# Performance work log

Hardware: AMD Instinct MI355X
Metric: run time of the kernel (lower is better)

## Reference

```python
import jax, jax.numpy as jnp
import numpy as np

H = 64  # hidden_dim

def _lstm_layer(x, Wih, Whh, bih, bhh):
    # x: [B,T,D]; Wih: [4H,D]; Whh: [4H,H]; biases: [4H]
    B = x.shape[0]
    xW = jnp.einsum('btd,gd->btg', x, Wih) + (bih + bhh)  # [B,T,4H], fold both biases
    xW = jnp.swapaxes(xW, 0, 1)  # [T,B,4H]
    h0 = jnp.zeros((B, H), x.dtype)
    c0 = jnp.zeros((B, H), x.dtype)

    def step(carry, g_x):
        h, c = carry
        gates = g_x + h @ Whh.T  # [B,4H]; torch gate order i,f,g,o
        i, f, g, o = jnp.split(gates, 4, axis=-1)
        i = jax.nn.sigmoid(i)
        f = jax.nn.sigmoid(f)
        g = jnp.tanh(g)
        o = jax.nn.sigmoid(o)
        c = f * c + i * g
        h = o * jnp.tanh(c)
        return (h, c), h

    (hT, cT), hs = jax.lax.scan(step, (h0, c0), xW)
    return jnp.swapaxes(hs, 0, 1), hT  # [B,T,H], [B,H]


def setup_inputs() -> dict:
    key = jax.random.key(0)
    ks = jax.random.split(key, 14)
    B, T, D = 2048, 1024, 1
    s = 1.0 / np.sqrt(H)  # torch LSTM/Linear init scale
    u = lambda k, shape: jax.random.uniform(k, shape, jnp.float32, -s, s)
    return {
        'x': jax.random.normal(ks[0], (B, T, D), jnp.float32),
        'Wih0': u(ks[1], (4 * H, D)),
        'Whh0': u(ks[2], (4 * H, H)),
        'bih0': u(ks[3], (4 * H,)),
        'bhh0': u(ks[4], (4 * H,)),
        'Wih1': u(ks[5], (4 * H, H)),
        'Whh1': u(ks[6], (4 * H, H)),
        'bih1': u(ks[7], (4 * H,)),
        'bhh1': u(ks[8], (4 * H,)),
        'Wc1': u(ks[9], (H // 2, H)),
        'bc1': u(ks[10], (H // 2,)),
        'Wc2': u(ks[11], (1, H // 2)),
        'bc2': u(ks[12], (1,)),
    }


def reference(x, Wih0, Whh0, bih0, bhh0, Wih1, Whh1, bih1, bhh1, Wc1, bc1, Wc2, bc2):
    # 2-layer unidirectional LSTM (dropout off at inference)
    h1_seq, _ = _lstm_layer(x, Wih0, Whh0, bih0, bhh0)
    _, h_n = _lstm_layer(h1_seq, Wih1, Whh1, bih1, bhh1)  # final hidden of top layer [B,H]
    # classifier head: Linear(H,H//2) -> ReLU -> Linear(H//2,1)
    hid = jax.nn.relu(h_n @ Wc1.T + bc1)
    logits = hid @ Wc2.T + bc2  # [B,1]
    return logits
```

## Files before the change

kernel.cpp:

```cpp
#include <hip/hip_runtime.h>

typedef _Float16 f16;
typedef _Float16 f16x8 __attribute__((ext_vector_type(8)));
typedef float    f32x4 __attribute__((ext_vector_type(4)));
typedef unsigned int       u32;
typedef unsigned long long u64;

#define HD    64
#define GW    16
#define NT    512
#define CHUNK 8
#define XCH   256
#define L2E   1.44269504088896340736f
#define L2E2  2.88539008177792681472f

#define BAR_LGKM() asm volatile("s_waitcnt lgkmcnt(0)\ns_barrier" ::: "memory")

#if __has_builtin(__builtin_amdgcn_exp2f)
#define EXP2(x) __builtin_amdgcn_exp2f(x)
#else
#define EXP2(x) __expf((x) * 0.69314718055994530942f)
#endif

__device__ __forceinline__ f32x4 MFMA(f16x8 a, f16x8 b, f32x4 c) {
    return __builtin_amdgcn_mfma_f32_16x16x32_f16(a, b, c, 0, 0, 0);
}
__device__ __forceinline__ int kinv(int k) {
    int kf = k >> 5, qk = (k >> 3) & 3, j = k & 7;
    int tile = (kf << 3) | (qk << 1) | (j & 1);
    return tile * 4 + (j >> 1);
}
__device__ __forceinline__ u32 packf16(f16 a, f16 b) {
    union { f16 h[2]; u32 u; } x; x.h[0] = a; x.h[1] = b; return x.u;
}
__device__ __forceinline__ u64 pollflag(u64* p, u64 need) {
    int guard = 0; u64 v;
    while ((v = __hip_atomic_load(p, __ATOMIC_RELAXED, __HIP_MEMORY_SCOPE_AGENT)) < need) {
        __builtin_amdgcn_s_sleep(2);
        if (++guard > (1 << 20)) break;
    }
    return v;
}

__device__ __forceinline__ void lstm_act(float gi, float gf, float gg, float go,
                                         float& cL, float& h) {
    float ef = EXP2(-gf);
    float fv = __builtin_amdgcn_rcpf(1.0f + ef);
    float ei = EXP2(-gi);
    float eg = EXP2(gg);
    float igL = fmaf(eg, L2E2, -L2E2) *
                __builtin_amdgcn_rcpf((1.0f + ei) * (eg + 1.0f));
    cL = fmaf(fv, cL, igL);
    float eo = EXP2(-go);
    float ec = EXP2(cL);
    h = (ec - 1.0f) * __builtin_amdgcn_rcpf((1.0f + eo) * (ec + 1.0f));
}

extern "C" __global__ void init_ws_k(u64* flags) {
    int i = blockIdx.x * 256 + threadIdx.x;
    if (i < 8192) flags[i] = 0;
}

extern "C" __global__ void __launch_bounds__(NT, 2)
lstm2_pair(const float* __restrict__ x,
           const float* __restrict__ Wih0, const float* __restrict__ Whh0,
           const float* __restrict__ bih0, const float* __restrict__ bhh0,
           const float* __restrict__ Wih1, const float* __restrict__ Whh1,
           const float* __restrict__ bih1, const float* __restrict__ bhh1,
           const float* __restrict__ Wc1,  const float* __restrict__ bc1,
           const float* __restrict__ Wc2,  const float* __restrict__ bc2,
           float* __restrict__ out, char* __restrict__ ws,
           int T, int groups, int slots)
{
    __shared__ __align__(16) f16 bBuf[2][2][64][8];
    __shared__ float xs[XCH][GW];
    __shared__ float hf[GW][HD];
    __shared__ float hid[GW][HD / 2];

    const int tid  = threadIdx.x;
    const int wave = tid >> 6;
    const int lane = tid & 63;
    const int q    = lane >> 4;
    const int n    = lane & 15;
    const int role  = blockIdx.x / groups;
    const int group = blockIdx.x % groups;
    const int b0    = group * GW;
    const int smask = slots - 1;

    u64* prodF = (u64*)(ws + (size_t)group * 128);
    u64* consF = (u64*)(ws + 32768 + (size_t)group * 128);
    char* ringG = ws + 65536 + (size_t)group * ((size_t)slots * 4096);

    { int* p = (int*)&bBuf[0][0][0][0];
      for (int i = tid; i < 1024; i += NT) p[i] = 0; }

    const int gA  = n & 3;
    const int tt0 = 2 * wave;
    const int kfL = wave >> 2;
    const int qk  = wave & 3;
    const int row = qk * 16 + n;
    const f32x4 z4 = {0.f, 0.f, 0.f, 0.f};
    const float scA = (gA == 2) ? L2E2 : L2E;

    if (role == 0) {
        f16x8 Ahi[4];
        f32x4 bias[2], wxv[2];
#pragma unroll
        for (int u = 0; u < 2; ++u) {
            const int tt = tt0 + u;
            const int rowA = gA * HD + tt * 4 + (n >> 2);
#pragma unroll
            for (int kf = 0; kf < 2; ++kf) {
                f16x8 hi;
#pragma unroll
                for (int j = 0; j < 8; ++j)
                    hi[j] = (f16)(Whh0[(size_t)rowA * HD + kinv(kf * 32 + q * 8 + j)] * scA);
                Ahi[u * 2 + kf] = hi;
            }
            const int uc = tt * 4 + q;
#pragma unroll
            for (int g = 0; g < 4; ++g) {
                float sg = (g == 2) ? L2E2 : L2E;
                bias[u][g] = (bih0[g * HD + uc] + bhh0[g * HD + uc]) * sg;
                wxv[u][g]  = Wih0[g * HD + uc] * sg;
            }
        }
        float c[2] = {0.f, 0.f};
        u64 cfcache = 0;
        __syncthreads();

#pragma unroll 1
        for (int t = 0; t < T; ++t) {
            if ((t & (CHUNK - 1)) == 1 && t > CHUNK) {
                asm volatile("s_waitcnt vmcnt(4)" ::: "memory");
                if (lane == 0)
                    __hip_atomic_fetch_add(prodF, 1ull,
                                           __ATOMIC_RELAXED, __HIP_MEMORY_SCOPE_AGENT);
            }
            if ((t & (XCH - 1)) == 0) {
                for (int i = tid; i < GW * XCH / 4; i += NT) {
                    int bb = i >> 6, t4 = (i & 63) * 4;
                    if (t + t4 < T) {
                        float4 v = *(const float4*)&x[(size_t)(b0 + bb) * T + t + t4];
                        xs[t4 + 0][bb] = v.x; xs[t4 + 1][bb] = v.y;
                        xs[t4 + 2][bb] = v.z; xs[t4 + 3][bb] = v.w;
                    }
                }
                BAR_LGKM();
            }
            if ((t & (CHUNK - 1)) == 0 && t + CHUNK > slots) {
                u64 need = (u64)(t + CHUNK - slots);
                if (tid == 0 && cfcache < need) cfcache = pollflag(consF, need);
                BAR_LGKM();
            }

            const int par = t & 1;
            f16x8 bh0 = *(const f16x8*)&bBuf[par][0][lane][0];
            f16x8 bh1 = *(const f16x8*)&bBuf[par][1][lane][0];
            float xv = xs[t & (XCH - 1)][n];
            float hq[2];
#pragma unroll
            for (int u = 0; u < 2; ++u) {
                f32x4 Ghi;
#pragma unroll
                for (int g = 0; g < 4; ++g) Ghi[g] = fmaf(wxv[u][g], xv, bias[u][g]);
                Ghi = MFMA(Ahi[u * 2 + 0], bh0, Ghi);
                Ghi = MFMA(Ahi[u * 2 + 1], bh1, Ghi);
                lstm_act(Ghi[0], Ghi[1], Ghi[2], Ghi[3], c[u], hq[u]);
            }
            u32 pH = packf16((f16)hq[0], (f16)hq[1]);
            *(u32*)&bBuf[par ^ 1][kfL][row][2 * q] = pH;
            char* sb = ringG + (size_t)(t & smask) * 4096;
            __hip_atomic_store((u32*)(sb + (kfL * 64 + row) * 16 + q * 4), pH,
                               __ATOMIC_RELAXED, __HIP_MEMORY_SCOPE_AGENT);
            BAR_LGKM();
        }
        asm volatile("s_waitcnt vmcnt(0)" ::: "memory");
        if (lane == 0)
            __hip_atomic_fetch_add(prodF, 1ull,
                                   __ATOMIC_RELAXED, __HIP_MEMORY_SCOPE_AGENT);
    } else {
        f16x8 Ahi[8];
        f32x4 bias[2];
#pragma unroll
        for (int u = 0; u < 2; ++u) {
            const int tt = tt0 + u;
            const int rowA = gA * HD + tt * 4 + (n >> 2);
#pragma unroll
            for (int kf = 0; kf < 4; ++kf) {
                f16x8 hi;
#pragma unroll
                for (int j = 0; j < 8; ++j)
                    hi[j] = (f16)(((kf < 2)
                        ? Wih1[(size_t)rowA * HD + kinv(kf * 32 + q * 8 + j)]
                        : Whh1[(size_t)rowA * HD + kinv((kf - 2) * 32 + q * 8 + j)]) * scA);
                Ahi[u * 4 + kf] = hi;
            }
            const int uc = tt * 4 + q;
#pragma unroll
            for (int g = 0; g < 4; ++g)
                bias[u][g] = (bih1[g * HD + uc] + bhh1[g * HD + uc])
                             * ((g == 2) ? L2E2 : L2E);
        }
        float c[2] = {0.f, 0.f};
        f16x8 pfh[2][2];

        auto loadslot = [&](int s, int buf) {
            char* sb = ringG + (size_t)(s & smask) * 4096 + (size_t)lane * 16;
#pragma unroll
            for (int kf = 0; kf < 2; ++kf) {
                union { u64 d[2]; f16x8 v; } Uh;
                u64* ph = (u64*)(sb + kf * 1024);
                Uh.d[0] = __hip_atomic_load(ph,     __ATOMIC_RELAXED, __HIP_MEMORY_SCOPE_AGENT);
                Uh.d[1] = __hip_atomic_load(ph + 1, __ATOMIC_RELAXED, __HIP_MEMORY_SCOPE_AGENT);
                pfh[buf][kf] = Uh.v;
            }
        };
        u64 pfcache = 0;
        __syncthreads();

#pragma unroll 1
        for (int cs = 0; cs < T; cs += CHUNK) {
            u64 need = (u64)((cs + 16 > T) ? T : cs + 16);
            if (tid == 0 && pfcache < need) pfcache = pollflag(prodF, need);
            BAR_LGKM();
            if (cs == 0) { loadslot(0, 0); loadslot(1, 1); }
#pragma unroll
            for (int cc = 0; cc < CHUNK; ++cc) {
                const int s = cs + cc;
                const int buf = s & 1, par = s & 1;
                f16x8 ch0 = *(const f16x8*)&bBuf[par][0][lane][0];
                f16x8 ch1 = *(const f16x8*)&bBuf[par][1][lane][0];
                float hq[2];
#pragma unroll
                for (int u = 0; u < 2; ++u) {
                    f32x4 GA = MFMA(Ahi[u * 4 + 0], pfh[buf][0], bias[u]);
                    GA = MFMA(Ahi[u * 4 + 1], pfh[buf][1], GA);
                    f32x4 GB = MFMA(Ahi[u * 4 + 2], ch0, z4);
                    GB = MFMA(Ahi[u * 4 + 3], ch1, GB);
                    lstm_act(GA[0] + GB[0], GA[1] + GB[1],
                             GA[2] + GB[2], GA[3] + GB[3], c[u], hq[u]);
                }
                if (s + 2 < T) loadslot(s + 2, buf);
                u32 pH = packf16((f16)hq[0], (f16)hq[1]);
                *(u32*)&bBuf[par ^ 1][kfL][row][2 * q] = pH;
                if (s == T - 1) {
                    hf[n][(tt0 + 0) * 4 + q] = hq[0];
                    hf[n][(tt0 + 1) * 4 + q] = hq[1];
                }
                BAR_LGKM();
            }
            if (tid == 0)
                __hip_atomic_store(consF, (u64)(cs + CHUNK),
                                   __ATOMIC_RELAXED, __HIP_MEMORY_SCOPE_AGENT);
        }

        __syncthreads();
        if (tid < GW * 32) {
            int nn = tid >> 5, m = tid & 31;
            float acc = bc1[m];
            const float* wr = Wc1 + m * HD;
#pragma unroll
            for (int k = 0; k < HD; ++k) acc += wr[k] * hf[nn][k];
            hid[nn][m] = fmaxf(acc, 0.0f);
        }
        __syncthreads();
        if (tid < GW) {
            float acc = bc2[0];
#pragma unroll
            for (int k = 0; k < HD / 2; ++k) acc += Wc2[k] * hid[tid][k];
            out[b0 + tid] = acc;
        }
    }
}

extern "C" void kernel_launch(void* const* d_in, const int* in_sizes, int n_in,
                              void* d_out, int out_size, void* d_ws, size_t ws_size,
                              hipStream_t stream) {
    const float* x    = (const float*)d_in[0];
    const float* Wih0 = (const float*)d_in[1];
    const float* Whh0 = (const float*)d_in[2];
    const float* bih0 = (const float*)d_in[3];
    const float* bhh0 = (const float*)d_in[4];
    const float* Wih1 = (const float*)d_in[5];
    const float* Whh1 = (const float*)d_in[6];
    const float* bih1 = (const float*)d_in[7];
    const float* bhh1 = (const float*)d_in[8];
    const float* Wc1  = (const float*)d_in[9];
    const float* bc1  = (const float*)d_in[10];
    const float* Wc2  = (const float*)d_in[11];
    const float* bc2  = (const float*)d_in[12];

    const int B = out_size;
    const int T = in_sizes[0] / B;
    const int groups = B / GW;

    int slots = 8;
    while (slots < 64 &&
           65536 + (size_t)groups * (size_t)(slots * 2) * 4096 <= ws_size)
        slots *= 2;

    hipLaunchKernelGGL(init_ws_k, dim3(32), dim3(256), 0, stream, (u64*)d_ws);
    hipLaunchKernelGGL(lstm2_pair, dim3(2 * groups), dim3(NT), 0, stream,
                       x, Wih0, Whh0, bih0, bhh0,
                       Wih1, Whh1, bih1, bhh1,
                       Wc1, bc1, Wc2, bc2,
                       (float*)d_out, (char*)d_ws, T, groups, slots);
}
```

Baseline: 550.0 us.

## Double threads per block so each wave handles one gate tile per step

The block grows from 512 to 1024 threads (16 waves), so each wave computes one 16-unit gate tile per timestep instead of two. This halves the serial MFMA and activation work per wave on the recurrent critical path. Hidden-state writes become 16-bit stores to LDS and to the global ring, and the producer flag now counts two increments per chunk because twice as many waves signal. The costs are fewer blocks per CU (launch bounds go from 2 to 1), a barrier across 16 waves every step, and narrower, more numerous stores.

```diff
diff --git a/kernel.cpp b/kernel.cpp
--- a/kernel.cpp
+++ b/kernel.cpp
@@ -4,11 +4,12 @@
 typedef _Float16 f16x8 __attribute__((ext_vector_type(8)));
 typedef float    f32x4 __attribute__((ext_vector_type(4)));
 typedef unsigned int       u32;
+typedef unsigned short     u16;
 typedef unsigned long long u64;
 
 #define HD    64
 #define GW    16
-#define NT    512
+#define NT    1024
 #define CHUNK 8
 #define XCH   256
 #define L2E   1.44269504088896340736f
@@ -29,9 +30,6 @@
     int kf = k >> 5, qk = (k >> 3) & 3, j = k & 7;
     int tile = (kf << 3) | (qk << 1) | (j & 1);
     return tile * 4 + (j >> 1);
-}
-__device__ __forceinline__ u32 packf16(f16 a, f16 b) {
-    union { f16 h[2]; u32 u; } x; x.h[0] = a; x.h[1] = b; return x.u;
 }
 __device__ __forceinline__ u64 pollflag(u64* p, u64 need) {
     int guard = 0; u64 v;
@@ -61,7 +59,7 @@
     if (i < 8192) flags[i] = 0;
 }
 
-extern "C" __global__ void __launch_bounds__(NT, 2)
+extern "C" __global__ void __launch_bounds__(NT, 1)
 lstm2_pair(const float* __restrict__ x,
            const float* __restrict__ Wih0, const float* __restrict__ Whh0,
            const float* __restrict__ bih0, const float* __restrict__ bhh0,
@@ -95,19 +93,17 @@
       for (int i = tid; i < 1024; i += NT) p[i] = 0; }
 
     const int gA  = n & 3;
-    const int tt0 = 2 * wave;
-    const int kfL = wave >> 2;
-    const int qk  = wave & 3;
-    const int row = qk * 16 + n;
+    const int tt  = wave;
+    const int kfP  = wave >> 3;
+    const int rowP = ((wave >> 1) & 3) * 16 + n;
+    const int jP   = 2 * q + (wave & 1);
     const f32x4 z4 = {0.f, 0.f, 0.f, 0.f};
     const float scA = (gA == 2) ? L2E2 : L2E;
 
     if (role == 0) {
-        f16x8 Ahi[4];
-        f32x4 bias[2], wxv[2];
-#pragma unroll
-        for (int u = 0; u < 2; ++u) {
-            const int tt = tt0 + u;
+        f16x8 Ahi[2];
+        f32x4 bias, wxv;
+        {
             const int rowA = gA * HD + tt * 4 + (n >> 2);
 #pragma unroll
             for (int kf = 0; kf < 2; ++kf) {
@@ -115,17 +111,17 @@
 #pragma unroll
                 for (int j = 0; j < 8; ++j)
                     hi[j] = (f16)(Whh0[(size_t)rowA * HD + kinv(kf * 32 + q * 8 + j)] * scA);
-                Ahi[u * 2 + kf] = hi;
+                Ahi[kf] = hi;
             }
             const int uc = tt * 4 + q;
 #pragma unroll
             for (int g = 0; g < 4; ++g) {
                 float sg = (g == 2) ? L2E2 : L2E;
-                bias[u][g] = (bih0[g * HD + uc] + bhh0[g * HD + uc]) * sg;
-                wxv[u][g]  = Wih0[g * HD + uc] * sg;
-            }
-        }
-        float c[2] = {0.f, 0.f};
+                bias[g] = (bih0[g * HD + uc] + bhh0[g * HD + uc]) * sg;
+                wxv[g]  = Wih0[g * HD + uc] * sg;
+            }
+        }
+        float c = 0.f;
         u64 cfcache = 0;
         __syncthreads();
 
@@ -138,13 +134,11 @@
                                            __ATOMIC_RELAXED, __HIP_MEMORY_SCOPE_AGENT);
             }
             if ((t & (XCH - 1)) == 0) {
-                for (int i = tid; i < GW * XCH / 4; i += NT) {
-                    int bb = i >> 6, t4 = (i & 63) * 4;
-                    if (t + t4 < T) {
-                        float4 v = *(const float4*)&x[(size_t)(b0 + bb) * T + t + t4];
-                        xs[t4 + 0][bb] = v.x; xs[t4 + 1][bb] = v.y;
-                        xs[t4 + 2][bb] = v.z; xs[t4 + 3][bb] = v.w;
-                    }
+                int bb = tid >> 6, t4 = (tid & 63) * 4;
+                if (t + t4 < T) {
+                    float4 v = *(const float4*)&x[(size_t)(b0 + bb) * T + t + t4];
+                    xs[t4 + 0][bb] = v.x; xs[t4 + 1][bb] = v.y;
+                    xs[t4 + 2][bb] = v.z; xs[t4 + 3][bb] = v.w;
                 }
                 BAR_LGKM();
             }
@@ -158,20 +152,17 @@
             f16x8 bh0 = *(const f16x8*)&bBuf[par][0][lane][0];
             f16x8 bh1 = *(const f16x8*)&bBuf[par][1][lane][0];
             float xv = xs[t & (XCH - 1)][n];
-            float hq[2];
-#pragma unroll
-            for (int u = 0; u < 2; ++u) {
-                f32x4 Ghi;
-#pragma unroll
-                for (int g = 0; g < 4; ++g) Ghi[g] = fmaf(wxv[u][g], xv, bias[u][g]);
-                Ghi = MFMA(Ahi[u * 2 + 0], bh0, Ghi);
-                Ghi = MFMA(Ahi[u * 2 + 1], bh1, Ghi);
-                lstm_act(Ghi[0], Ghi[1], Ghi[2], Ghi[3], c[u], hq[u]);
-            }
-            u32 pH = packf16((f16)hq[0], (f16)hq[1]);
-            *(u32*)&bBuf[par ^ 1][kfL][row][2 * q] = pH;
+            f32x4 Ghi;
+#pragma unroll
+            for (int g = 0; g < 4; ++g) Ghi[g] = fmaf(wxv[g], xv, bias[g]);
+            Ghi = MFMA(Ahi[0], bh0, Ghi);
+            Ghi = MFMA(Ahi[1], bh1, Ghi);
+            float hq;
+            lstm_act(Ghi[0], Ghi[1], Ghi[2], Ghi[3], c, hq);
+            union { f16 h; u16 u; } hv; hv.h = (f16)hq;
+            bBuf[par ^ 1][kfP][rowP][jP] = hv.h;
             char* sb = ringG + (size_t)(t & smask) * 4096;
-            __hip_atomic_store((u32*)(sb + (kfL * 64 + row) * 16 + q * 4), pH,
+            __hip_atomic_store((u16*)(sb + (kfP * 64 + rowP) * 16 + jP * 2), hv.u,
                                __ATOMIC_RELAXED, __HIP_MEMORY_SCOPE_AGENT);
             BAR_LGKM();
         }
@@ -180,11 +171,9 @@
             __hip_atomic_fetch_add(prodF, 1ull,
                                    __ATOMIC_RELAXED, __HIP_MEMORY_SCOPE_AGENT);
     } else {
-        f16x8 Ahi[8];
-        f32x4 bias[2];
-#pragma unroll
-        for (int u = 0; u < 2; ++u) {
-            const int tt = tt0 + u;
+        f16x8 Ahi[4];
+        f32x4 bias;
+        {
             const int rowA = gA * HD + tt * 4 + (n >> 2);
 #pragma unroll
             for (int kf = 0; kf < 4; ++kf) {
@@ -194,15 +183,15 @@
                     hi[j] = (f16)(((kf < 2)
                         ? Wih1[(size_t)rowA * HD + kinv(kf * 32 + q * 8 + j)]
                         : Whh1[(size_t)rowA * HD + kinv((kf - 2) * 32 + q * 8 + j)]) * scA);
-                Ahi[u * 4 + kf] = hi;
+                Ahi[kf] = hi;
             }
             const int uc = tt * 4 + q;
 #pragma unroll
             for (int g = 0; g < 4; ++g)
-                bias[u][g] = (bih1[g * HD + uc] + bhh1[g * HD + uc])
-                             * ((g == 2) ? L2E2 : L2E);
-        }
-        float c[2] = {0.f, 0.f};
+                bias[g] = (bih1[g * HD + uc] + bhh1[g * HD + uc])
+                          * ((g == 2) ? L2E2 : L2E);
+        }
+        float c = 0.f;
         f16x8 pfh[2][2];
 
         auto loadslot = [&](int s, int buf) {
@@ -221,7 +210,7 @@
 
 #pragma unroll 1
         for (int cs = 0; cs < T; cs += CHUNK) {
-            u64 need = (u64)((cs + 16 > T) ? T : cs + 16);
+            u64 need = (u64)((2 * cs + 32 > 2 * T) ? 2 * T : 2 * cs + 32);
             if (tid == 0 && pfcache < need) pfcache = pollflag(prodF, need);
             BAR_LGKM();
             if (cs == 0) { loadslot(0, 0); loadslot(1, 1); }
@@ -231,23 +220,17 @@
                 const int buf = s & 1, par = s & 1;
                 f16x8 ch0 = *(const f16x8*)&bBuf[par][0][lane][0];
                 f16x8 ch1 = *(const f16x8*)&bBuf[par][1][lane][0];
-                float hq[2];
-#pragma unroll
-                for (int u = 0; u < 2; ++u) {
-                    f32x4 GA = MFMA(Ahi[u * 4 + 0], pfh[buf][0], bias[u]);
-                    GA = MFMA(Ahi[u * 4 + 1], pfh[buf][1], GA);
-                    f32x4 GB = MFMA(Ahi[u * 4 + 2], ch0, z4);
-                    GB = MFMA(Ahi[u * 4 + 3], ch1, GB);
-                    lstm_act(GA[0] + GB[0], GA[1] + GB[1],
-                             GA[2] + GB[2], GA[3] + GB[3], c[u], hq[u]);
-                }
+                f32x4 GA = MFMA(Ahi[0], pfh[buf][0], bias);
+                GA = MFMA(Ahi[1], pfh[buf][1], GA);
+                f32x4 GB = MFMA(Ahi[2], ch0, z4);
+                GB = MFMA(Ahi[3], ch1, GB);
+                float hq;
+                lstm_act(GA[0] + GB[0], GA[1] + GB[1],
+                         GA[2] + GB[2], GA[3] + GB[3], c, hq);
                 if (s + 2 < T) loadslot(s + 2, buf);
-                u32 pH = packf16((f16)hq[0], (f16)hq[1]);
-                *(u32*)&bBuf[par ^ 1][kfL][row][2 * q] = pH;
-                if (s == T - 1) {
-                    hf[n][(tt0 + 0) * 4 + q] = hq[0];
-                    hf[n][(tt0 + 1) * 4 + q] = hq[1];
-                }
+                bBuf[par ^ 1][kfP][rowP][jP] = (f16)hq;
+                if (s == T - 1)
+                    hf[n][tt * 4 + q] = hq;
                 BAR_LGKM();
             }
             if (tid == 0)
```

Result: slower. 703.0 us (+27.8%).
